# Optimization experiments

Hardware: AMD Instinct MI355X
Metric: run time of the kernel (lower is better)

The kernel has to match this reference:

```python
import jax, jax.numpy as jnp
import numpy as np

B, T, E = 1024, 200, 64
NU, NM, NC = 100000, 1000000, 1000
D_LAU_IN = 8 * E      # 512
D_MLP_IN = 7 * E      # 448
EPS = 1e-5
NEG = -2.0 ** 31


def setup_inputs() -> dict:
    key = jax.random.key(0)
    ks = jax.random.split(key, 32)
    f = lambda k, shape, s=0.05: (jax.random.normal(k, shape, dtype=jnp.float32) * s)
    inp = {
        "uid": jax.random.randint(ks[0], (B,), 0, NU, dtype=jnp.int32),
        "mid": jax.random.randint(ks[1], (B,), 0, NM, dtype=jnp.int32),
        "cat": jax.random.randint(ks[2], (B,), 0, NC, dtype=jnp.int32),
        "historical_mid": jax.random.randint(ks[3], (B, T), 0, NM, dtype=jnp.int32),
        "historical_cat": jax.random.randint(ks[4], (B, T), 0, NC, dtype=jnp.int32),
        "mask": jax.random.randint(ks[5], (B, T), 0, 2, dtype=jnp.int32),
        # embedding tables
        "user_table": f(ks[6], (NU, E), 0.1),
        "mat_table": f(ks[7], (NM, E), 0.1),
        "cat_table": f(ks[8], (NC, E), 0.1),
        # LocalActivationUnit: Linear(512,256)->Sigmoid->Linear(256,128)->Sigmoid->Linear(128,1)
        "lau_w1": f(ks[9], (D_LAU_IN, 256)), "lau_b1": f(ks[10], (256,)),
        "lau_w2": f(ks[11], (256, 128)),     "lau_b2": f(ks[12], (128,)),
        "lau_w3": f(ks[13], (128, 1)),       "lau_b3": f(ks[14], (1,)),
        # MLP: BN(448)->Linear(448,512)->BN->LeakyReLU(0.1)->Linear(512,256)->BN->LeakyReLU->Linear(256,2)
        "bn0_g": jnp.ones((D_MLP_IN,), jnp.float32), "bn0_b": jnp.zeros((D_MLP_IN,), jnp.float32),
        "mlp_w1": f(ks[15], (D_MLP_IN, 512)), "mlp_b1": f(ks[16], (512,)),
        "bn1_g": jnp.ones((512,), jnp.float32), "bn1_b": jnp.zeros((512,), jnp.float32),
        "mlp_w2": f(ks[17], (512, 256)),      "mlp_b2": f(ks[18], (256,)),
        "bn2_g": jnp.ones((256,), jnp.float32), "bn2_b": jnp.zeros((256,), jnp.float32),
        "mlp_w3": f(ks[19], (256, 2)),        "mlp_b3": f(ks[20], (2,)),
    }
    return inp


def _bn(x, g, b):
    # torch BatchNorm1d in training mode: batch mean, biased variance
    mu = jnp.mean(x, axis=0)
    var = jnp.var(x, axis=0)
    return (x - mu) * jax.lax.rsqrt(var + EPS) * g + b


def reference(uid, mid, cat, historical_mid, historical_cat, mask,
              user_table, mat_table, cat_table,
              lau_w1, lau_b1, lau_w2, lau_b2, lau_w3, lau_b3,
              bn0_g, bn0_b, mlp_w1, mlp_b1, bn1_g, bn1_b,
              mlp_w2, mlp_b2, bn2_g, bn2_b, mlp_w3, mlp_b3):
    u = user_table[uid]                                             # [B,E]
    cur = jnp.concatenate([mat_table[mid], cat_table[cat]], axis=1)  # [B,2E]
    hist = jnp.concatenate([mat_table[historical_mid],
                            cat_table[historical_cat]], axis=2)      # [B,T,2E]
    maskf = mask.astype(hist.dtype)                                  # [B,T]

    # Local activation unit
    cur_e = jnp.broadcast_to(cur[:, None, :], hist.shape)            # [B,T,2E]
    comb = jnp.concatenate([cur_e, hist, cur_e - hist, cur_e * hist], axis=2)  # [B,T,8E]
    h = jax.nn.sigmoid(comb @ lau_w1 + lau_b1)
    h = jax.nn.sigmoid(h @ lau_w2 + lau_b2)
    aw = (h @ lau_w3 + lau_b3)[..., 0]                               # [B,T]
    masked = jnp.where(mask == 1, aw, jnp.asarray(NEG, aw.dtype))
    scores = jax.nn.softmax(masked, axis=-1) * maskf                 # [B,T]
    lau = jnp.einsum('bt,bte->be', scores, hist)                     # [B,2E]

    # masked mean of history
    hsum = jnp.einsum('bt,bte->be', maskf, hist)
    hmean = hsum / jnp.sum(maskf, axis=1, keepdims=True)

    x = jnp.concatenate([u, cur, lau, hmean], axis=-1)               # [B,7E]
    x = _bn(x, bn0_g, bn0_b)
    x = jax.nn.leaky_relu(_bn(x @ mlp_w1 + mlp_b1, bn1_g, bn1_b), 0.1)
    x = jax.nn.leaky_relu(_bn(x @ mlp_w2 + mlp_b2, bn2_g, bn2_b), 0.1)
    return x @ mlp_w3 + mlp_b3                                        # [B,2]
```

## Files before the change

kernel.cpp:

```cpp
#include <hip/hip_runtime.h>

#define BB 1024
#define TT 200
#define MROWS (BB*TT)

typedef unsigned short u16;
typedef __attribute__((ext_vector_type(8))) short bf16x8;
typedef __attribute__((ext_vector_type(4))) float f32x4;

__device__ __forceinline__ u16 f2bf(float f) {
  unsigned u = __float_as_uint(f);
  u += 0x7fff + ((u >> 16) & 1);
  return (u16)(u >> 16);
}
__device__ __forceinline__ float bf2f(u16 h) {
  return __uint_as_float(((unsigned)h) << 16);
}

__global__ void prep_weights(const float* __restrict__ w1, const float* __restrict__ w2,
                             u16* __restrict__ WpT, float* __restrict__ Wq,
                             u16* __restrict__ W2T) {
  int i = blockIdx.x * 256 + threadIdx.x;
  if (i < 65536) {
    int n = i >> 8, k = i & 255;
    float v;
    if (k < 128) v = w1[(128 + k) * 256 + n] - w1[(256 + k) * 256 + n];
    else         v = w1[(384 + (k - 128)) * 256 + n];
    WpT[n * 256 + k] = f2bf(v);
  } else if (i < 98304) {
    int j = i - 65536;
    int k = j >> 8, jc = j & 255;
    Wq[j] = w1[k * 256 + jc] + w1[(256 + k) * 256 + jc];
  } else if (i < 131072) {
    int j = i - 98304;
    int n = j >> 8, k = j & 255;
    W2T[j] = f2bf(w2[k * 128 + n]);
  }
}

__global__ __launch_bounds__(256) void prep_batch(
    const int* __restrict__ mid, const int* __restrict__ cat,
    const float* __restrict__ mat_table, const float* __restrict__ cat_table,
    const float* __restrict__ lau_b1, const float* __restrict__ Wq,
    float* __restrict__ cur, float* __restrict__ bias1p) {
  int b = blockIdx.x, tid = threadIdx.x;
  __shared__ float curL[128];
  if (tid < 64)        curL[tid] = mat_table[(long)mid[b] * 64 + tid];
  else if (tid < 128)  curL[tid] = cat_table[(long)cat[b] * 64 + (tid - 64)];
  __syncthreads();
  if (tid < 128) cur[b * 128 + tid] = curL[tid];
  float s = lau_b1[tid];
  for (int k = 0; k < 128; ++k) s += curL[k] * Wq[k * 256 + tid];
  bias1p[b * 256 + tid] = s;
}

__global__ __launch_bounds__(256) void lau_fused(
    const int* __restrict__ hmid, const int* __restrict__ hcat,
    const float* __restrict__ mat_table, const float* __restrict__ cat_table,
    const float* __restrict__ cur, const float* __restrict__ bias1p,
    const u16* __restrict__ WpT, const u16* __restrict__ W2T,
    const float* __restrict__ b2, const float* __restrict__ w3,
    const float* __restrict__ b3,
    u16* __restrict__ Xh, float* __restrict__ AW) {
  __shared__ __align__(16) u16 Al[64 * 264];
  __shared__ float awp[4][64];
  int tid = threadIdx.x, wave = tid >> 6, l = tid & 63;
  int q = l >> 4, r16 = l & 15;
  long mBase = (long)blockIdx.x * 64;

  for (int i = tid; i < 2048; i += 256) {
    int r = i >> 5, c4 = i & 31;
    long bt = mBase + r;
    int b = (int)(bt / TT);
    int e0 = c4 * 4;
    float4 hv;
    if (e0 < 64) hv = *(const float4*)(mat_table + (long)hmid[bt] * 64 + e0);
    else         hv = *(const float4*)(cat_table + (long)hcat[bt] * 64 + (e0 - 64));
    float4 cv = *(const float4*)(cur + b * 128 + e0);
    u16 hb[4] = {f2bf(hv.x), f2bf(hv.y), f2bf(hv.z), f2bf(hv.w)};
    u16 pb[4] = {f2bf(hv.x * cv.x), f2bf(hv.y * cv.y), f2bf(hv.z * cv.z), f2bf(hv.w * cv.w)};
    *(ushort4*)(Al + r * 264 + e0)       = *(ushort4*)hb;
    *(ushort4*)(Al + r * 264 + 128 + e0) = *(ushort4*)pb;
    *(ushort4*)(Xh + bt * 128 + e0)      = *(ushort4*)hb;
  }
  __syncthreads();

  f32x4 acc1[4][4] = {};
  const u16* wp1 = WpT + ((long)(wave * 64 + r16)) * 256 + q * 8;
  #pragma unroll
  for (int ki = 0; ki < 8; ++ki) {
    bf16x8 a[4];
    #pragma unroll
    for (int mt = 0; mt < 4; ++mt)
      a[mt] = *(const bf16x8*)(Al + (mt * 16 + r16) * 264 + ki * 32 + q * 8);
    #pragma unroll
    for (int nt = 0; nt < 4; ++nt) {
      bf16x8 bq = *(const bf16x8*)(wp1 + nt * (16 * 256) + ki * 32);
      #pragma unroll
      for (int mt = 0; mt < 4; ++mt)
        acc1[mt][nt] = __builtin_amdgcn_mfma_f32_16x16x32_bf16(a[mt], bq, acc1[mt][nt], 0, 0, 0);
    }
  }
  __syncthreads();
  #pragma unroll
  for (int mt = 0; mt < 4; ++mt)
    #pragma unroll
    for (int r = 0; r < 4; ++r) {
      int row = mt * 16 + q * 4 + r;
      int bidx = (int)((mBase + row) / TT);
      const float* bp = bias1p + (long)bidx * 256;
      #pragma unroll
      for (int nt = 0; nt < 4; ++nt) {
        int col = wave * 64 + nt * 16 + r16;
        float z = acc1[mt][nt][r] + bp[col];
        Al[row * 264 + col] = f2bf(1.f / (1.f + __expf(-z)));
      }
    }
  __syncthreads();

  f32x4 acc2[4][2] = {};
  const u16* wp2 = W2T + ((long)(wave * 32 + r16)) * 256 + q * 8;
  #pragma unroll
  for (int ki = 0; ki < 8; ++ki) {
    bf16x8 a[4];
    #pragma unroll
    for (int mt = 0; mt < 4; ++mt)
      a[mt] = *(const bf16x8*)(Al + (mt * 16 + r16) * 264 + ki * 32 + q * 8);
    #pragma unroll
    for (int nt = 0; nt < 2; ++nt) {
      bf16x8 bq = *(const bf16x8*)(wp2 + nt * (16 * 256) + ki * 32);
      #pragma unroll
      for (int mt = 0; mt < 4; ++mt)
        acc2[mt][nt] = __builtin_amdgcn_mfma_f32_16x16x32_bf16(a[mt], bq, acc2[mt][nt], 0, 0, 0);
    }
  }
  float rp[4][4];
  #pragma unroll
  for (int mt = 0; mt < 4; ++mt)
    #pragma unroll
    for (int r = 0; r < 4; ++r) rp[mt][r] = 0.f;
  #pragma unroll
  for (int nt = 0; nt < 2; ++nt) {
    int col = wave * 32 + nt * 16 + r16;
    float b2v = b2[col], w3v = w3[col];
    #pragma unroll
    for (int mt = 0; mt < 4; ++mt)
      #pragma unroll
      for (int r = 0; r < 4; ++r) {
        float z = acc2[mt][nt][r] + b2v;
        rp[mt][r] += w3v / (1.f + __expf(-z));
      }
  }
  #pragma unroll
  for (int off = 1; off < 16; off <<= 1)
    #pragma unroll
    for (int mt = 0; mt < 4; ++mt)
      #pragma unroll
      for (int r = 0; r < 4; ++r)
        rp[mt][r] += __shfl_xor(rp[mt][r], off, 16);
  if (r16 == 0)
    #pragma unroll
    for (int mt = 0; mt < 4; ++mt)
      #pragma unroll
      for (int r = 0; r < 4; ++r)
        awp[wave][mt * 16 + q * 4 + r] = rp[mt][r];
  __syncthreads();
  if (tid < 64)
    AW[mBase + tid] = awp[0][tid] + awp[1][tid] + awp[2][tid] + awp[3][tid] + b3[0];
}

__global__ __launch_bounds__(256) void softmax_pool(
    const float* __restrict__ AW, const int* __restrict__ mask,
    const int* __restrict__ uid, const float* __restrict__ user_table,
    const float* __restrict__ cur, const u16* __restrict__ Xh,
    float* __restrict__ Xmlp) {
  int b = blockIdx.x, tid = threadIdx.x;
  __shared__ float red[256];
  __shared__ float sc[TT], mkf[TT];
  __shared__ float ps[512];
  int mk = 0;
  float masked = -3.0e38f;
  if (tid < TT) {
    mk = mask[b * TT + tid];
    masked = mk ? AW[b * TT + tid] : -2147483648.0f;
  }
  red[tid] = masked; __syncthreads();
  for (int s = 128; s > 0; s >>= 1) { if (tid < s) red[tid] = fmaxf(red[tid], red[tid + s]); __syncthreads(); }
  float mx = red[0]; __syncthreads();
  float ev = (tid < TT) ? __expf(masked - mx) : 0.f;
  red[tid] = ev; __syncthreads();
  for (int s = 128; s > 0; s >>= 1) { if (tid < s) red[tid] += red[tid + s]; __syncthreads(); }
  float denom = red[0]; __syncthreads();
  red[tid] = (tid < TT) ? (float)mk : 0.f; __syncthreads();
  for (int s = 128; s > 0; s >>= 1) { if (tid < s) red[tid] += red[tid + s]; __syncthreads(); }
  float cnt = red[0]; __syncthreads();
  if (tid < TT) { sc[tid] = (ev / denom) * (float)mk; mkf[tid] = (float)mk; }
  __syncthreads();
  int c = tid & 127, p = tid >> 7;
  const u16* xb = Xh + (long)b * TT * 128 + c;
  float sL = 0.f, sH = 0.f;
  for (int t = p; t < TT; t += 2) {
    float hv = bf2f(xb[(long)t * 128]);
    sL += sc[t] * hv;
    sH += mkf[t] * hv;
  }
  ps[tid] = sL; ps[256 + tid] = sH;
  __syncthreads();
  if (tid < 128) {
    float lau  = ps[tid] + ps[tid + 128];
    float hsum = ps[256 + tid] + ps[256 + tid + 128];
    Xmlp[b * 448 + 192 + tid] = lau;
    Xmlp[b * 448 + 320 + tid] = hsum / cnt;
  } else {
    int j = tid - 128;
    Xmlp[b * 448 + 64 + j] = cur[b * 128 + j];
    if (j < 64) Xmlp[b * 448 + j] = user_table[(long)uid[b] * 64 + j];
  }
}

__global__ __launch_bounds__(256) void colstats(const float* __restrict__ X, int cols,
                                                float* __restrict__ psum,
                                                float* __restrict__ psq) {
  int cg = blockIdx.x, rc = blockIdx.y;
  int c = threadIdx.x & 63, ty = threadIdx.x >> 6;
  int col = cg * 64 + c;
  float s = 0.f, ss = 0.f;
  for (int i = 0; i < 16; ++i) {
    int r = rc * 64 + ty + i * 4;
    float v = X[(long)r * cols + col];
    s += v; ss += v * v;
  }
  __shared__ float s1[256], s2[256];
  s1[threadIdx.x] = s; s2[threadIdx.x] = ss;
  __syncthreads();
  if (ty == 0) {
    s  = s1[c] + s1[c + 64] + s1[c + 128] + s1[c + 192];
    ss = s2[c] + s2[c + 64] + s2[c + 128] + s2[c + 192];
    psum[rc * cols + col] = s;
    psq [rc * cols + col] = ss;
  }
}

template <bool LEAKY>
__global__ __launch_bounds__(256) void gemm_bn(
    const float* __restrict__ A, int K,
    const float* __restrict__ psumA, const float* __restrict__ psqA,
    const float* __restrict__ g, const float* __restrict__ bta,
    const float* __restrict__ W, const float* __restrict__ bias, int N,
    float* __restrict__ C, float* __restrict__ psumC, float* __restrict__ psqC) {
  __shared__ float As[16][65], Bs[16][65];
  __shared__ float scK[512], shK[512];
  __shared__ float colS[16][64], colQ[16][64];
  int tid = threadIdx.x;
  for (int j = tid; j < K; j += 256) {
    float s = 0.f, ss = 0.f;
    for (int rc = 0; rc < 16; ++rc) { s += psumA[rc * K + j]; ss += psqA[rc * K + j]; }
    float mu = s * (1.f / 1024.f), var = ss * (1.f / 1024.f) - mu * mu;
    float scv = rsqrtf(var + 1e-5f) * g[j];
    scK[j] = scv; shK[j] = bta[j] - mu * scv;
  }
  __syncthreads();
  int m0 = blockIdx.x * 64, n0 = blockIdx.y * 64;
  int tx = tid & 15, ty = tid >> 4;
  float acc[4][4] = {};
  for (int k0 = 0; k0 < K; k0 += 16) {
    __syncthreads();
    for (int i = tid; i < 1024; i += 256) {
      int m = i >> 4, k = i & 15;
      float v = A[(long)(m0 + m) * K + k0 + k] * scK[k0 + k] + shK[k0 + k];
      if (LEAKY) v = v > 0.f ? v : 0.1f * v;
      As[k][m] = v;
    }
    for (int i = tid; i < 1024; i += 256) {
      int k = i >> 6, n = i & 63;
      Bs[k][n] = W[(long)(k0 + k) * N + n0 + n];
    }
    __syncthreads();
    for (int k = 0; k < 16; ++k) {
      float a[4], bq[4];
      for (int ii = 0; ii < 4; ++ii) a[ii]  = As[k][ty * 4 + ii];
      for (int jj = 0; jj < 4; ++jj) bq[jj] = Bs[k][tx * 4 + jj];
      for (int ii = 0; ii < 4; ++ii)
        for (int jj = 0; jj < 4; ++jj) acc[ii][jj] += a[ii] * bq[jj];
    }
  }
  float cs4[4], cq4[4];
  for (int jj = 0; jj < 4; ++jj) {
    int n = n0 + tx * 4 + jj;
    float bv = bias[n];
    float cs = 0.f, cq = 0.f;
    for (int ii = 0; ii < 4; ++ii) {
      float val = acc[ii][jj] + bv;
      C[(long)(m0 + ty * 4 + ii) * N + n] = val;
      cs += val; cq += val * val;
    }
    cs4[jj] = cs; cq4[jj] = cq;
  }
  __syncthreads();
  for (int jj = 0; jj < 4; ++jj) {
    colS[ty][tx * 4 + jj] = cs4[jj];
    colQ[ty][tx * 4 + jj] = cq4[jj];
  }
  __syncthreads();
  if (tid < 64) {
    float s = 0.f, ss = 0.f;
    for (int t = 0; t < 16; ++t) { s += colS[t][tid]; ss += colQ[t][tid]; }
    psumC[blockIdx.x * N + n0 + tid] = s;
    psqC [blockIdx.x * N + n0 + tid] = ss;
  }
}

__global__ __launch_bounds__(256) void final_out(
    const float* __restrict__ y2,
    const float* __restrict__ psum2, const float* __restrict__ psq2,
    const float* __restrict__ g, const float* __restrict__ bta,
    const float* __restrict__ w3, const float* __restrict__ b3,
    float* __restrict__ out) {
  __shared__ float sc2[256], sh2[256];
  __shared__ float p0[256], p1[256];
  int tid = threadIdx.x;
  {
    float s = 0.f, ss = 0.f;
    for (int rc = 0; rc < 16; ++rc) { s += psum2[rc * 256 + tid]; ss += psq2[rc * 256 + tid]; }
    float mu = s * (1.f / 1024.f), var = ss * (1.f / 1024.f) - mu * mu;
    float scv = rsqrtf(var + 1e-5f) * g[tid];
    sc2[tid] = scv; sh2[tid] = bta[tid] - mu * scv;
  }
  __syncthreads();
  int row = blockIdx.x * 64 + (tid >> 2), q = tid & 3;
  const float* yr = y2 + (long)row * 256;
  float a0 = 0.f, a1 = 0.f;
  for (int k = q * 64; k < q * 64 + 64; ++k) {
    float v = yr[k] * sc2[k] + sh2[k];
    v = v > 0.f ? v : 0.1f * v;
    a0 += v * w3[2 * k];
    a1 += v * w3[2 * k + 1];
  }
  p0[tid] = a0; p1[tid] = a1;
  __syncthreads();
  if (q == 0) {
    out[row * 2 + 0] = p0[tid] + p0[tid + 1] + p0[tid + 2] + p0[tid + 3] + b3[0];
    out[row * 2 + 1] = p1[tid] + p1[tid + 1] + p1[tid + 2] + p1[tid + 3] + b3[1];
  }
}


extern "C" void kernel_launch(void* const* d_in, const int* in_sizes, int n_in,
                              void* d_out, int out_size, void* d_ws, size_t ws_size,
                              hipStream_t stream) {
  const int* uid  = (const int*)d_in[0];
  const int* mid  = (const int*)d_in[1];
  const int* cat  = (const int*)d_in[2];
  const int* hmid = (const int*)d_in[3];
  const int* hcat = (const int*)d_in[4];
  const int* mask = (const int*)d_in[5];
  const float* user_table = (const float*)d_in[6];
  const float* mat_table  = (const float*)d_in[7];
  const float* cat_table  = (const float*)d_in[8];
  const float* lau_w1 = (const float*)d_in[9];
  const float* lau_b1 = (const float*)d_in[10];
  const float* lau_w2 = (const float*)d_in[11];
  const float* lau_b2 = (const float*)d_in[12];
  const float* lau_w3 = (const float*)d_in[13];
  const float* lau_b3 = (const float*)d_in[14];
  const float* bn0_g = (const float*)d_in[15];
  const float* bn0_b = (const float*)d_in[16];
  const float* mlp_w1 = (const float*)d_in[17];
  const float* mlp_b1 = (const float*)d_in[18];
  const float* bn1_g = (const float*)d_in[19];
  const float* bn1_b = (const float*)d_in[20];
  const float* mlp_w2 = (const float*)d_in[21];
  const float* mlp_b2 = (const float*)d_in[22];
  const float* bn2_g = (const float*)d_in[23];
  const float* bn2_b = (const float*)d_in[24];
  const float* mlp_w3 = (const float*)d_in[25];
  const float* mlp_b3 = (const float*)d_in[26];
  float* out = (float*)d_out;

  char* w = (char*)d_ws;
  size_t off = 0;
  auto take = [&](size_t bytes) { size_t o = off; off += (bytes + 255) & ~(size_t)255; return o; };
  u16*   Xh     = (u16*)  (w + take((size_t)MROWS * 128 * 2));
  float* AW     = (float*)(w + take((size_t)MROWS * 4));
  float* cur    = (float*)(w + take((size_t)BB * 128 * 4));
  float* bias1p = (float*)(w + take((size_t)BB * 256 * 4));
  float* xmlp   = (float*)(w + take((size_t)BB * 448 * 4));
  float* y1     = (float*)(w + take((size_t)BB * 512 * 4));
  float* y2     = (float*)(w + take((size_t)BB * 256 * 4));
  u16*   WpT    = (u16*)  (w + take(256 * 256 * 2));
  float* Wq     = (float*)(w + take(128 * 256 * 4));
  u16*   W2T    = (u16*)  (w + take(128 * 256 * 2));
  float* psum0  = (float*)(w + take(16 * 448 * 4));
  float* psq0   = (float*)(w + take(16 * 448 * 4));
  float* psum1  = (float*)(w + take(16 * 512 * 4));
  float* psq1   = (float*)(w + take(16 * 512 * 4));
  float* psum2  = (float*)(w + take(16 * 256 * 4));
  float* psq2   = (float*)(w + take(16 * 256 * 4));

  prep_weights<<<512, 256, 0, stream>>>(lau_w1, lau_w2, WpT, Wq, W2T);
  prep_batch<<<BB, 256, 0, stream>>>(mid, cat, mat_table, cat_table, lau_b1, Wq, cur, bias1p);
  lau_fused<<<MROWS / 64, 256, 0, stream>>>(hmid, hcat, mat_table, cat_table, cur, bias1p,
                                            WpT, W2T, lau_b2, lau_w3, lau_b3, Xh, AW);
  softmax_pool<<<BB, 256, 0, stream>>>(AW, mask, uid, user_table, cur, Xh, xmlp);
  {
    dim3 g(448 / 64, 16);
    colstats<<<g, 256, 0, stream>>>(xmlp, 448, psum0, psq0);
  }
  {
    dim3 g(16, 512 / 64);
    gemm_bn<false><<<g, 256, 0, stream>>>(xmlp, 448, psum0, psq0, bn0_g, bn0_b,
                                          mlp_w1, mlp_b1, 512, y1, psum1, psq1);
  }
  {
    dim3 g(16, 256 / 64);
    gemm_bn<true><<<g, 256, 0, stream>>>(y1, 512, psum1, psq1, bn1_g, bn1_b,
                                         mlp_w2, mlp_b2, 256, y2, psum2, psq2);
  }
  final_out<<<16, 256, 0, stream>>>(y2, psum2, psq2, bn2_g, bn2_b, mlp_w3, mlp_b3, out);
}
```

Measured before the change: 748.1 us.

## Prefetch MFMA weight fragments, hoist biases, use fast rcp sigmoid, widen pooling loads

```diff
diff --git a/kernel.cpp b/kernel.cpp
--- a/kernel.cpp
+++ b/kernel.cpp
@@ -15,6 +15,9 @@
 }
 __device__ __forceinline__ float bf2f(u16 h) {
   return __uint_as_float(((unsigned)h) << 16);
+}
+__device__ __forceinline__ float fast_sigmoid(float z) {
+  return __builtin_amdgcn_rcpf(1.f + __expf(-z));
 }
 
 __global__ void prep_weights(const float* __restrict__ w1, const float* __restrict__ w2,
@@ -54,7 +57,7 @@
   bias1p[b * 256 + tid] = s;
 }
 
-__global__ __launch_bounds__(256) void lau_fused(
+__global__ __launch_bounds__(256, 4) void lau_fused(
     const int* __restrict__ hmid, const int* __restrict__ hcat,
     const float* __restrict__ mat_table, const float* __restrict__ cat_table,
     const float* __restrict__ cur, const float* __restrict__ bias1p,
@@ -67,6 +70,23 @@
   int tid = threadIdx.x, wave = tid >> 6, l = tid & 63;
   int q = l >> 4, r16 = l & 15;
   long mBase = (long)blockIdx.x * 64;
+  int b0 = (int)(mBase / TT), b1 = (int)((mBase + 63) / TT);
+  long thresh = (long)(b0 + 1) * TT;
+
+  float bias_a[4], bias_b[4];
+  #pragma unroll
+  for (int nt = 0; nt < 4; ++nt) {
+    int col = wave * 64 + nt * 16 + r16;
+    bias_a[nt] = bias1p[(long)b0 * 256 + col];
+    bias_b[nt] = bias1p[(long)b1 * 256 + col];
+  }
+  float b2v[2], w3v[2];
+  #pragma unroll
+  for (int nt = 0; nt < 2; ++nt) {
+    int col = wave * 32 + nt * 16 + r16;
+    b2v[nt] = b2[col]; w3v[nt] = w3[col];
+  }
+  float b3v = b3[0];
 
   for (int i = tid; i < 2048; i += 256) {
     int r = i >> 5, c4 = i & 31;
@@ -85,8 +105,12 @@
   }
   __syncthreads();
 
+  const u16* wp1 = WpT + ((long)(wave * 64 + r16)) * 256 + q * 8;
+  bf16x8 bfr[4];
+  #pragma unroll
+  for (int nt = 0; nt < 4; ++nt)
+    bfr[nt] = *(const bf16x8*)(wp1 + nt * 4096);
   f32x4 acc1[4][4] = {};
-  const u16* wp1 = WpT + ((long)(wave * 64 + r16)) * 256 + q * 8;
   #pragma unroll
   for (int ki = 0; ki < 8; ++ki) {
     bf16x8 a[4];
@@ -95,10 +119,12 @@
       a[mt] = *(const bf16x8*)(Al + (mt * 16 + r16) * 264 + ki * 32 + q * 8);
     #pragma unroll
     for (int nt = 0; nt < 4; ++nt) {
-      bf16x8 bq = *(const bf16x8*)(wp1 + nt * (16 * 256) + ki * 32);
+      bf16x8 bu = bfr[nt];
+      if (ki < 7)
+        bfr[nt] = *(const bf16x8*)(wp1 + nt * 4096 + (ki + 1) * 32);
       #pragma unroll
       for (int mt = 0; mt < 4; ++mt)
-        acc1[mt][nt] = __builtin_amdgcn_mfma_f32_16x16x32_bf16(a[mt], bq, acc1[mt][nt], 0, 0, 0);
+        acc1[mt][nt] = __builtin_amdgcn_mfma_f32_16x16x32_bf16(a[mt], bu, acc1[mt][nt], 0, 0, 0);
     }
   }
   __syncthreads();
@@ -107,19 +133,21 @@
     #pragma unroll
     for (int r = 0; r < 4; ++r) {
       int row = mt * 16 + q * 4 + r;
-      int bidx = (int)((mBase + row) / TT);
-      const float* bp = bias1p + (long)bidx * 256;
+      bool hi = (mBase + row) >= thresh;
       #pragma unroll
       for (int nt = 0; nt < 4; ++nt) {
         int col = wave * 64 + nt * 16 + r16;
-        float z = acc1[mt][nt][r] + bp[col];
-        Al[row * 264 + col] = f2bf(1.f / (1.f + __expf(-z)));
+        float z = acc1[mt][nt][r] + (hi ? bias_b[nt] : bias_a[nt]);
+        Al[row * 264 + col] = f2bf(fast_sigmoid(z));
       }
     }
   __syncthreads();
 
+  const u16* wp2 = W2T + ((long)(wave * 32 + r16)) * 256 + q * 8;
+  bf16x8 b2f[2];
+  b2f[0] = *(const bf16x8*)(wp2);
+  b2f[1] = *(const bf16x8*)(wp2 + 4096);
   f32x4 acc2[4][2] = {};
-  const u16* wp2 = W2T + ((long)(wave * 32 + r16)) * 256 + q * 8;
   #pragma unroll
   for (int ki = 0; ki < 8; ++ki) {
     bf16x8 a[4];
@@ -128,10 +156,12 @@
       a[mt] = *(const bf16x8*)(Al + (mt * 16 + r16) * 264 + ki * 32 + q * 8);
     #pragma unroll
     for (int nt = 0; nt < 2; ++nt) {
-      bf16x8 bq = *(const bf16x8*)(wp2 + nt * (16 * 256) + ki * 32);
+      bf16x8 bu = b2f[nt];
+      if (ki < 7)
+        b2f[nt] = *(const bf16x8*)(wp2 + nt * 4096 + (ki + 1) * 32);
       #pragma unroll
       for (int mt = 0; mt < 4; ++mt)
-        acc2[mt][nt] = __builtin_amdgcn_mfma_f32_16x16x32_bf16(a[mt], bq, acc2[mt][nt], 0, 0, 0);
+        acc2[mt][nt] = __builtin_amdgcn_mfma_f32_16x16x32_bf16(a[mt], bu, acc2[mt][nt], 0, 0, 0);
     }
   }
   float rp[4][4];
@@ -141,14 +171,12 @@
     for (int r = 0; r < 4; ++r) rp[mt][r] = 0.f;
   #pragma unroll
   for (int nt = 0; nt < 2; ++nt) {
-    int col = wave * 32 + nt * 16 + r16;
-    float b2v = b2[col], w3v = w3[col];
     #pragma unroll
     for (int mt = 0; mt < 4; ++mt)
       #pragma unroll
       for (int r = 0; r < 4; ++r) {
-        float z = acc2[mt][nt][r] + b2v;
-        rp[mt][r] += w3v / (1.f + __expf(-z));
+        float z = acc2[mt][nt][r] + b2v[nt];
+        rp[mt][r] += w3v[nt] * fast_sigmoid(z);
       }
   }
   #pragma unroll
@@ -166,7 +194,7 @@
         awp[wave][mt * 16 + q * 4 + r] = rp[mt][r];
   __syncthreads();
   if (tid < 64)
-    AW[mBase + tid] = awp[0][tid] + awp[1][tid] + awp[2][tid] + awp[3][tid] + b3[0];
+    AW[mBase + tid] = awp[0][tid] + awp[1][tid] + awp[2][tid] + awp[3][tid] + b3v;
 }
 
 __global__ __launch_bounds__(256) void softmax_pool(
@@ -175,42 +203,50 @@
     const float* __restrict__ cur, const u16* __restrict__ Xh,
     float* __restrict__ Xmlp) {
   int b = blockIdx.x, tid = threadIdx.x;
-  __shared__ float red[256];
+  __shared__ float redA[256], redB[256];
   __shared__ float sc[TT], mkf[TT];
-  __shared__ float ps[512];
+  __shared__ float pl0[256], pl1[256], ph0[256], ph1[256];
   int mk = 0;
   float masked = -3.0e38f;
   if (tid < TT) {
     mk = mask[b * TT + tid];
     masked = mk ? AW[b * TT + tid] : -2147483648.0f;
   }
-  red[tid] = masked; __syncthreads();
-  for (int s = 128; s > 0; s >>= 1) { if (tid < s) red[tid] = fmaxf(red[tid], red[tid + s]); __syncthreads(); }
-  float mx = red[0]; __syncthreads();
+  redA[tid] = masked; __syncthreads();
+  for (int s = 128; s > 0; s >>= 1) { if (tid < s) redA[tid] = fmaxf(redA[tid], redA[tid + s]); __syncthreads(); }
+  float mx = redA[0]; __syncthreads();
   float ev = (tid < TT) ? __expf(masked - mx) : 0.f;
-  red[tid] = ev; __syncthreads();
-  for (int s = 128; s > 0; s >>= 1) { if (tid < s) red[tid] += red[tid + s]; __syncthreads(); }
-  float denom = red[0]; __syncthreads();
-  red[tid] = (tid < TT) ? (float)mk : 0.f; __syncthreads();
-  for (int s = 128; s > 0; s >>= 1) { if (tid < s) red[tid] += red[tid + s]; __syncthreads(); }
-  float cnt = red[0]; __syncthreads();
-  if (tid < TT) { sc[tid] = (ev / denom) * (float)mk; mkf[tid] = (float)mk; }
-  __syncthreads();
-  int c = tid & 127, p = tid >> 7;
-  const u16* xb = Xh + (long)b * TT * 128 + c;
-  float sL = 0.f, sH = 0.f;
-  for (int t = p; t < TT; t += 2) {
-    float hv = bf2f(xb[(long)t * 128]);
-    sL += sc[t] * hv;
-    sH += mkf[t] * hv;
-  }
-  ps[tid] = sL; ps[256 + tid] = sH;
+  redA[tid] = ev; redB[tid] = (tid < TT) ? (float)mk : 0.f;
+  __syncthreads();
+  for (int s = 128; s > 0; s >>= 1) {
+    if (tid < s) { redA[tid] += redA[tid + s]; redB[tid] += redB[tid + s]; }
+    __syncthreads();
+  }
+  float rdenom = __builtin_amdgcn_rcpf(redA[0]);
+  float cnt = redB[0]; __syncthreads();
+  if (tid < TT) { sc[tid] = ev * rdenom * (float)mk; mkf[tid] = (float)mk; }
+  __syncthreads();
+  int cp = tid & 63, p = tid >> 6;
+  const u16* xb = Xh + (long)b * TT * 128 + 2 * cp;
+  float sL0 = 0.f, sL1 = 0.f, sH0 = 0.f, sH1 = 0.f;
+  for (int t = p; t < TT; t += 4) {
+    unsigned v = *(const unsigned*)(xb + (long)t * 128);
+    float h0 = bf2f((u16)(v & 0xffff));
+    float h1 = bf2f((u16)(v >> 16));
+    float s = sc[t], m = mkf[t];
+    sL0 += s * h0; sL1 += s * h1;
+    sH0 += m * h0; sH1 += m * h1;
+  }
+  pl0[tid] = sL0; pl1[tid] = sL1; ph0[tid] = sH0; ph1[tid] = sH1;
   __syncthreads();
   if (tid < 128) {
-    float lau  = ps[tid] + ps[tid + 128];
-    float hsum = ps[256 + tid] + ps[256 + tid + 128];
+    int c2 = tid >> 1, part = tid & 1;
+    const float* PL = part ? pl1 : pl0;
+    const float* PH = part ? ph1 : ph0;
+    float lau = PL[c2] + PL[64 + c2] + PL[128 + c2] + PL[192 + c2];
+    float hs  = PH[c2] + PH[64 + c2] + PH[128 + c2] + PH[192 + c2];
     Xmlp[b * 448 + 192 + tid] = lau;
-    Xmlp[b * 448 + 320 + tid] = hsum / cnt;
+    Xmlp[b * 448 + 320 + tid] = hs * __builtin_amdgcn_rcpf(cnt);
   } else {
     int j = tid - 128;
     Xmlp[b * 448 + 64 + j] = cur[b * 128 + j];
```

Measured after the change: 709.4 us. -5.2%, faster.
